# Kernel optimization log

Hardware: AMD Instinct MI355X
Metric: run time of the kernel (lower is better)

## Reference

```python
import jax, jax.numpy as jnp
import numpy as np

B, S, D, H, DFF, L = 8192, 9, 3, 3, 2048, 3
HD = D // H  # head dim = 1
EPS = 1e-5


def _ln(x, g, b):
    m = jnp.mean(x, axis=-1, keepdims=True)
    v = jnp.var(x, axis=-1, keepdims=True)
    return (x - m) * jax.lax.rsqrt(v + EPS) * g + b


def _encoder_layer(h, Wqkv, bqkv, Wo, bo, g1, b1, W1, bf1, W2, bf2, g2, b2):
    # h: [B,S,D]; post-norm TransformerEncoderLayer (PyTorch defaults, eval mode)
    qkv = jnp.einsum('bsd,ed->bse', h, Wqkv) + bqkv      # [B,S,3D]
    q, k, v = jnp.split(qkv, 3, axis=-1)
    Bv = h.shape[0]
    q = q.reshape(Bv, S, H, HD) * (1.0 / np.sqrt(HD))
    k = k.reshape(Bv, S, H, HD)
    v = v.reshape(Bv, S, H, HD)
    attn = jax.nn.softmax(jnp.einsum('bqhd,bkhd->bhqk', q, k), axis=-1)
    o = jnp.einsum('bhqk,bkhd->bqhd', attn, v).reshape(Bv, S, D)
    o = jnp.einsum('bsd,od->bso', o, Wo) + bo
    h = _ln(h + o, g1, b1)
    ff = jax.nn.relu(jnp.einsum('bsd,fd->bsf', h, W1) + bf1)  # [B,S,DFF]
    ff = jnp.einsum('bsf,df->bsd', ff, W2) + bf2
    return _ln(h + ff, g2, b2)


def setup_inputs() -> dict:
    key = jax.random.key(0)
    ks = jax.random.split(key, 8)
    sc = 0.3
    return {
        'x': jax.random.normal(ks[0], (B, S * D), dtype=jnp.float32),
        'Wqkv': sc * jax.random.normal(ks[1], (L, 3 * D, D), dtype=jnp.float32),
        'bqkv': jnp.zeros((L, 3 * D), jnp.float32),
        'Wo': sc * jax.random.normal(ks[2], (L, D, D), dtype=jnp.float32),
        'bo': jnp.zeros((L, D), jnp.float32),
        'g1': jnp.ones((L, D), jnp.float32),
        'beta1': jnp.zeros((L, D), jnp.float32),
        'W1': sc * jax.random.normal(ks[3], (L, DFF, D), dtype=jnp.float32),
        'bf1': jnp.zeros((L, DFF), jnp.float32),
        'W2': (sc / np.sqrt(DFF)) * jax.random.normal(ks[4], (L, D, DFF), dtype=jnp.float32),
        'bf2': jnp.zeros((L, D), jnp.float32),
        'g2': jnp.ones((L, D), jnp.float32),
        'beta2': jnp.zeros((L, D), jnp.float32),
        'W': jax.random.normal(ks[5], (D, S), dtype=jnp.float32),
    }


def reference(x, Wqkv, bqkv, Wo, bo, g1, beta1, W1, bf1, W2, bf2, g2, beta2, W):
    h = x.reshape(-1, S, D)                      # split 27-dim state into 9 tokens of 3
    for i in range(L):
        h = _encoder_layer(h, Wqkv[i], bqkv[i], Wo[i], bo[i], g1[i], beta1[i],
                           W1[i], bf1[i], W2[i], bf2[i], g2[i], beta2[i])
    # per-token matmul with W then softmax over the 9 logits (dim=0 of each 9-vector)
    z = jax.nn.softmax(jnp.einsum('bsd,dn->bsn', h, W), axis=-1)  # [B,S,9]
    u = jnp.prod(z, axis=1)                      # elementwise product over 9 tokens
    return jax.nn.softmax(u, axis=-1)            # [B,9] action probabilities
```

## Files before the change

### kernel.cpp

```cpp
#include <hip/hip_runtime.h>
#include <math.h>


constexpr int S   = 9;
constexpr int D   = 3;
constexpr int DFF = 2048;
constexpr int L   = 3;
constexpr int G   = 16;
constexpr int BLK = 256;
constexpr int BPB = BLK / G;
constexpr int FPT = DFF / G;
constexpr int PPT = FPT / 2;
constexpr float EPS = 1e-5f;

typedef float v2f __attribute__((ext_vector_type(2)));
typedef float v4f __attribute__((ext_vector_type(4)));

__device__ __forceinline__ v2f pk_fma(v2f a, v2f b, v2f c) {
    v2f d;
    asm("v_pk_fma_f32 %0, %1, %2, %3" : "=v"(d) : "v"(a), "v"(b), "v"(c));
    return d;
}

__launch_bounds__(BLK, 2)
__global__ void tf_policy_kernel(const float* __restrict__ x,
                                 const float* __restrict__ Wqkv,
                                 const float* __restrict__ bqkv,
                                 const float* __restrict__ Wo,
                                 const float* __restrict__ bo,
                                 const float* __restrict__ g1,
                                 const float* __restrict__ be1,
                                 const float* __restrict__ W1,
                                 const float* __restrict__ bf1,
                                 const float* __restrict__ W2,
                                 const float* __restrict__ bf2,
                                 const float* __restrict__ g2,
                                 const float* __restrict__ be2,
                                 const float* __restrict__ Wfin,
                                 float* __restrict__ out)
{
    __shared__ v4f s_a[DFF / 2];
    __shared__ v4f s_b[DFF / 2];
    __shared__ v4f s_c[DFF / 2];
    __shared__ v2f s_d[DFF / 2];

    const int tid = threadIdx.x;
    const int grp = tid >> 4;
    const int sub = tid & 15;
    const int b   = blockIdx.x * BPB + grp;

    float h[S][D];
    {
        const float* xr = x + (size_t)b * (S * D);
        #pragma unroll
        for (int s = 0; s < S; ++s)
            #pragma unroll
            for (int d = 0; d < D; ++d)
                h[s][d] = xr[s * D + d];
    }

    for (int l = 0; l < L; ++l) {
        __syncthreads();
        {
            const float* w1p = W1  + (size_t)l * DFF * D;
            const float* b1p = bf1 + (size_t)l * DFF;
            const float* w2p = W2  + (size_t)l * D * DFF;
            const v2f* w1v = (const v2f*)w1p;
            const v2f* b1v = (const v2f*)b1p;
            const v2f* c0v = (const v2f*)w2p;
            const v2f* c1v = (const v2f*)(w2p + DFF);
            const v2f* c2v = (const v2f*)(w2p + 2 * DFF);
            for (int p = tid; p < DFF / 2; p += BLK) {
                v2f r0 = w1v[3 * p];
                v2f r1 = w1v[3 * p + 1];
                v2f r2 = w1v[3 * p + 2];
                v2f bb = b1v[p];
                v2f c0 = c0v[p];
                v2f c1 = c1v[p];
                v2f c2 = c2v[p];
                s_a[p] = (v4f){r0.x, r1.y, r0.y, r2.x};
                s_b[p] = (v4f){r1.x, r2.y, bb.x, bb.y};
                s_c[p] = (v4f){c0.x, c0.y, c1.x, c1.y};
                s_d[p] = c2;
            }
        }
        __syncthreads();

        const float* wq = Wqkv + (size_t)l * (3 * D) * D;
        const float* bq = bqkv + (size_t)l * (3 * D);
        float o[S][D];
        #pragma unroll
        for (int hh = 0; hh < 3; ++hh) {
            float q[S], k[S], v[S];
            #pragma unroll
            for (int s = 0; s < S; ++s) {
                q[s] = fmaf(wq[hh * 3 + 0], h[s][0],
                       fmaf(wq[hh * 3 + 1], h[s][1],
                       fmaf(wq[hh * 3 + 2], h[s][2], bq[hh])));
                k[s] = fmaf(wq[(3 + hh) * 3 + 0], h[s][0],
                       fmaf(wq[(3 + hh) * 3 + 1], h[s][1],
                       fmaf(wq[(3 + hh) * 3 + 2], h[s][2], bq[3 + hh])));
                v[s] = fmaf(wq[(6 + hh) * 3 + 0], h[s][0],
                       fmaf(wq[(6 + hh) * 3 + 1], h[s][1],
                       fmaf(wq[(6 + hh) * 3 + 2], h[s][2], bq[6 + hh])));
            }
            #pragma unroll
            for (int qs = 0; qs < S; ++qs) {
                float sc[S];
                float m = -1e30f;
                #pragma unroll
                for (int ks = 0; ks < S; ++ks) {
                    sc[ks] = q[qs] * k[ks];
                    m = fmaxf(m, sc[ks]);
                }
                float sum = 0.f, av = 0.f;
                #pragma unroll
                for (int ks = 0; ks < S; ++ks) {
                    float e = __expf(sc[ks] - m);
                    sum += e;
                    av = fmaf(e, v[ks], av);
                }
                o[qs][hh] = av / sum;
            }
        }

        {
            const float* wo  = Wo  + (size_t)l * D * D;
            const float* bop = bo  + (size_t)l * D;
            const float* gp  = g1  + (size_t)l * D;
            const float* bp  = be1 + (size_t)l * D;
            #pragma unroll
            for (int s = 0; s < S; ++s) {
                float t[D];
                #pragma unroll
                for (int dd = 0; dd < D; ++dd)
                    t[dd] = h[s][dd] + bop[dd] +
                            fmaf(wo[dd * 3 + 0], o[s][0],
                            fmaf(wo[dd * 3 + 1], o[s][1],
                                 wo[dd * 3 + 2] * o[s][2]));
                float m  = (t[0] + t[1] + t[2]) * (1.f / 3.f);
                float d0 = t[0] - m, d1 = t[1] - m, d2 = t[2] - m;
                float va = (d0 * d0 + d1 * d1 + d2 * d2) * (1.f / 3.f);
                float r  = rsqrtf(va + EPS);
                h[s][0] = fmaf(d0 * r, gp[0], bp[0]);
                h[s][1] = fmaf(d1 * r, gp[1], bp[1]);
                h[s][2] = fmaf(d2 * r, gp[2], bp[2]);
            }
        }

        v2f hb[S][D];
        #pragma unroll
        for (int s = 0; s < S; ++s)
            #pragma unroll
            for (int d = 0; d < D; ++d)
                hb[s][d] = (v2f){h[s][d], h[s][d]};

        v2f acc2[S][D];
        #pragma unroll
        for (int s = 0; s < S; ++s)
            #pragma unroll
            for (int d = 0; d < D; ++d)
                acc2[s][d] = (v2f){0.f, 0.f};

        #pragma unroll 2
        for (int i = 0; i < PPT; ++i) {
            const int p = i * G + sub;
            const v4f A  = s_a[p];
            const v4f Bv = s_b[p];
            const v4f C  = s_c[p];
            const v2f Dz = s_d[p];
            const v2f w1x = A.xy,  w1y = A.zw;
            const v2f w1z = Bv.xy, w1b = Bv.zw;
            const v2f w2x = C.xy,  w2y = C.zw;
            #pragma unroll
            for (int s = 0; s < S; ++s) {
                v2f t = pk_fma(w1x, hb[s][0],
                        pk_fma(w1y, hb[s][1],
                        pk_fma(w1z, hb[s][2], w1b)));
                t.x = fmaxf(t.x, 0.f);
                t.y = fmaxf(t.y, 0.f);
                acc2[s][0] = pk_fma(C.xy, t, acc2[s][0]);
                acc2[s][1] = pk_fma(w2y, t, acc2[s][1]);
                acc2[s][2] = pk_fma(Dz, t, acc2[s][2]);
                (void)w2x;
            }
        }

        float acc[S][D];
        #pragma unroll
        for (int s = 0; s < S; ++s)
            #pragma unroll
            for (int d = 0; d < D; ++d)
                acc[s][d] = acc2[s][d].x + acc2[s][d].y;

        #pragma unroll
        for (int mask = 1; mask < G; mask <<= 1) {
            #pragma unroll
            for (int s = 0; s < S; ++s)
                #pragma unroll
                for (int d = 0; d < D; ++d)
                    acc[s][d] += __shfl_xor(acc[s][d], mask, 64);
        }

        {
            const float* b2p = bf2 + (size_t)l * D;
            const float* gp  = g2  + (size_t)l * D;
            const float* bp  = be2 + (size_t)l * D;
            #pragma unroll
            for (int s = 0; s < S; ++s) {
                float t[D];
                #pragma unroll
                for (int dd = 0; dd < D; ++dd)
                    t[dd] = h[s][dd] + acc[s][dd] + b2p[dd];
                float m  = (t[0] + t[1] + t[2]) * (1.f / 3.f);
                float d0 = t[0] - m, d1 = t[1] - m, d2 = t[2] - m;
                float va = (d0 * d0 + d1 * d1 + d2 * d2) * (1.f / 3.f);
                float r  = rsqrtf(va + EPS);
                h[s][0] = fmaf(d0 * r, gp[0], bp[0]);
                h[s][1] = fmaf(d1 * r, gp[1], bp[1]);
                h[s][2] = fmaf(d2 * r, gp[2], bp[2]);
            }
        }
    }

    if (sub == 0) {
        float u[S];
        #pragma unroll
        for (int n = 0; n < S; ++n) u[n] = 1.f;
        #pragma unroll
        for (int s = 0; s < S; ++s) {
            float z[S];
            float m = -1e30f;
            #pragma unroll
            for (int n = 0; n < S; ++n) {
                z[n] = fmaf(h[s][0], Wfin[0 * S + n],
                       fmaf(h[s][1], Wfin[1 * S + n],
                            h[s][2] * Wfin[2 * S + n]));
                m = fmaxf(m, z[n]);
            }
            float sum = 0.f;
            #pragma unroll
            for (int n = 0; n < S; ++n) { z[n] = __expf(z[n] - m); sum += z[n]; }
            float inv = 1.f / sum;
            #pragma unroll
            for (int n = 0; n < S; ++n) u[n] *= z[n] * inv;
        }
        float m = -1e30f;
        #pragma unroll
        for (int n = 0; n < S; ++n) m = fmaxf(m, u[n]);
        float e[S];
        float sum = 0.f;
        #pragma unroll
        for (int n = 0; n < S; ++n) { e[n] = __expf(u[n] - m); sum += e[n]; }
        float inv = 1.f / sum;
        float* op = out + (size_t)b * S;
        #pragma unroll
        for (int n = 0; n < S; ++n) op[n] = e[n] * inv;
    }
}

extern "C" void kernel_launch(void* const* d_in, const int* in_sizes, int n_in,
                              void* d_out, int out_size, void* d_ws, size_t ws_size,
                              hipStream_t stream)
{
    const float* x    = (const float*)d_in[0];
    const float* Wqkv = (const float*)d_in[1];
    const float* bqkv = (const float*)d_in[2];
    const float* Wo   = (const float*)d_in[3];
    const float* bo   = (const float*)d_in[4];
    const float* g1   = (const float*)d_in[5];
    const float* be1  = (const float*)d_in[6];
    const float* W1   = (const float*)d_in[7];
    const float* bf1  = (const float*)d_in[8];
    const float* W2   = (const float*)d_in[9];
    const float* bf2  = (const float*)d_in[10];
    const float* g2   = (const float*)d_in[11];
    const float* be2  = (const float*)d_in[12];
    const float* Wfin = (const float*)d_in[13];
    float* out = (float*)d_out;

    const int B = in_sizes[0] / (S * D);
    const int nblocks = B / BPB;

    tf_policy_kernel<<<nblocks, BLK, 0, stream>>>(
        x, Wqkv, bqkv, Wo, bo, g1, be1, W1, bf1, W2, bf2, g2, be2, Wfin, out);
}
```

Measured before the change: 119.8 us.

## Split attention rows across the 16 lanes of each group via shared memory

Before, every one of the 16 lanes in a group computed all 27 (head, query) attention rows redundantly. Now each lane computes at most two rows, writes them to a padded shared buffer, and after a block barrier every lane reads back the full attention output. The launch-bounds occupancy hint drops from 2 to 1 block per SIMD, and the FFN loop unroll goes from 2 to 4. This trades redundant attention math for extra LDS traffic and a barrier per layer, and the lower occupancy hint may allow more registers at the cost of less latency hiding.

```diff
diff --git a/kernel.cpp b/kernel.cpp
--- a/kernel.cpp
+++ b/kernel.cpp
@@ -11,6 +11,8 @@
 constexpr int BPB = BLK / G;
 constexpr int FPT = DFF / G;
 constexpr int PPT = FPT / 2;
+constexpr int NROW = 27;
+constexpr int ATT_STRIDE = 33;
 constexpr float EPS = 1e-5f;
 
 typedef float v2f __attribute__((ext_vector_type(2)));
@@ -22,7 +24,7 @@
     return d;
 }
 
-__launch_bounds__(BLK, 2)
+__launch_bounds__(BLK, 1)
 __global__ void tf_policy_kernel(const float* __restrict__ x,
                                  const float* __restrict__ Wqkv,
                                  const float* __restrict__ bqkv,
@@ -43,6 +45,7 @@
     __shared__ v4f s_b[DFF / 2];
     __shared__ v4f s_c[DFF / 2];
     __shared__ v2f s_d[DFF / 2];
+    __shared__ float s_att[BPB * ATT_STRIDE];
 
     const int tid = threadIdx.x;
     const int grp = tid >> 4;
@@ -88,29 +91,30 @@
 
         const float* wq = Wqkv + (size_t)l * (3 * D) * D;
         const float* bq = bqkv + (size_t)l * (3 * D);
-        float o[S][D];
-        #pragma unroll
-        for (int hh = 0; hh < 3; ++hh) {
-            float q[S], k[S], v[S];
-            #pragma unroll
-            for (int s = 0; s < S; ++s) {
-                q[s] = fmaf(wq[hh * 3 + 0], h[s][0],
-                       fmaf(wq[hh * 3 + 1], h[s][1],
-                       fmaf(wq[hh * 3 + 2], h[s][2], bq[hh])));
-                k[s] = fmaf(wq[(3 + hh) * 3 + 0], h[s][0],
-                       fmaf(wq[(3 + hh) * 3 + 1], h[s][1],
-                       fmaf(wq[(3 + hh) * 3 + 2], h[s][2], bq[3 + hh])));
-                v[s] = fmaf(wq[(6 + hh) * 3 + 0], h[s][0],
-                       fmaf(wq[(6 + hh) * 3 + 1], h[s][1],
-                       fmaf(wq[(6 + hh) * 3 + 2], h[s][2], bq[6 + hh])));
-            }
-            #pragma unroll
-            for (int qs = 0; qs < S; ++qs) {
+        #pragma unroll
+        for (int rr = 0; rr < 2; ++rr) {
+            const int r = sub + rr * 16;
+            if (r < NROW) {
+                const int hh = r / 9;
+                const int qs = r % 9;
+                float q = fmaf(wq[hh * 3 + 0], h[qs][0],
+                          fmaf(wq[hh * 3 + 1], h[qs][1],
+                          fmaf(wq[hh * 3 + 2], h[qs][2], bq[hh])));
+                float kk[S], vv[S];
+                #pragma unroll
+                for (int s = 0; s < S; ++s) {
+                    kk[s] = fmaf(wq[(3 + hh) * 3 + 0], h[s][0],
+                            fmaf(wq[(3 + hh) * 3 + 1], h[s][1],
+                            fmaf(wq[(3 + hh) * 3 + 2], h[s][2], bq[3 + hh])));
+                    vv[s] = fmaf(wq[(6 + hh) * 3 + 0], h[s][0],
+                            fmaf(wq[(6 + hh) * 3 + 1], h[s][1],
+                            fmaf(wq[(6 + hh) * 3 + 2], h[s][2], bq[6 + hh])));
+                }
                 float sc[S];
                 float m = -1e30f;
                 #pragma unroll
                 for (int ks = 0; ks < S; ++ks) {
-                    sc[ks] = q[qs] * k[ks];
+                    sc[ks] = q * kk[ks];
                     m = fmaxf(m, sc[ks]);
                 }
                 float sum = 0.f, av = 0.f;
@@ -118,13 +122,21 @@
                 for (int ks = 0; ks < S; ++ks) {
                     float e = __expf(sc[ks] - m);
                     sum += e;
-                    av = fmaf(e, v[ks], av);
+                    av = fmaf(e, vv[ks], av);
                 }
-                o[qs][hh] = av / sum;
-            }
-        }
+                s_att[grp * ATT_STRIDE + r] = av / sum;
+            }
+        }
+        __syncthreads();
 
         {
+            float o[S][D];
+            #pragma unroll
+            for (int hh = 0; hh < D; ++hh)
+                #pragma unroll
+                for (int s = 0; s < S; ++s)
+                    o[s][hh] = s_att[grp * ATT_STRIDE + hh * 9 + s];
+
             const float* wo  = Wo  + (size_t)l * D * D;
             const float* bop = bo  + (size_t)l * D;
             const float* gp  = g1  + (size_t)l * D;
@@ -162,7 +174,7 @@
             for (int d = 0; d < D; ++d)
                 acc2[s][d] = (v2f){0.f, 0.f};
 
-        #pragma unroll 2
+        #pragma unroll 4
         for (int i = 0; i < PPT; ++i) {
             const int p = i * G + sub;
             const v4f A  = s_a[p];
@@ -179,10 +191,9 @@
                         pk_fma(w1z, hb[s][2], w1b)));
                 t.x = fmaxf(t.x, 0.f);
                 t.y = fmaxf(t.y, 0.f);
-                acc2[s][0] = pk_fma(C.xy, t, acc2[s][0]);
+                acc2[s][0] = pk_fma(w2x, t, acc2[s][0]);
                 acc2[s][1] = pk_fma(w2y, t, acc2[s][1]);
                 acc2[s][2] = pk_fma(Dz, t, acc2[s][2]);
-                (void)w2x;
             }
         }
 
```

Result: faster. 110.0 us (-8.2%).
